# Kernel tuning notes

Hardware: AMD Instinct MI355X
Metric: run time of the kernel (lower is better)

The kernel has to match this reference:

```python
import jax, jax.numpy as jnp
import numpy as np
from jax.scipy.special import logsumexp

H = 256      # hidden_dim
K = 128      # num_clusters
SPW = 64     # states_per_word
C = K * SPW  # 8192 total states
V = 10000    # vocab
N, T = 16, 256
NEG = -1e9   # finite -inf for masking (avoids NaN rows in log_softmax)


def _residual(x, w1, b1, w2, b2):
    # ResidualLayerOld: relu(lin2(relu(lin1(x))) + x)
    h = jax.nn.relu(x @ w1.T + b1)
    return jax.nn.relu(h @ w2.T + b2 + x)


def _emb(ec, es):
    # Factored StateEmbedding: state s -> cluster_emb[s // SPW] + offset_emb[s % SPW]
    return (ec[:, None, :] + es[None, :, :]).reshape(-1, ec.shape[-1])  # [C, H]


def setup_inputs() -> dict:
    key = jax.random.key(0)
    ks = jax.random.split(key, 32)
    d = {}
    d["text"] = jax.random.randint(ks[0], (N, T), 0, V)
    d["word2cluster"] = jax.random.randint(ks[1], (V,), 0, K)
    i = 2
    for nm in ["start", "state", "next", "pre"]:
        d[nm + "_emb_c"] = jax.random.normal(ks[i], (K, H), jnp.float32) * 0.02; i += 1
        d[nm + "_emb_s"] = jax.random.normal(ks[i], (SPW, H), jnp.float32) * 0.02; i += 1
    for nm in ["start_res", "trans_res", "term_res"]:
        d[nm + "_w1"] = jax.random.normal(ks[i], (H, H), jnp.float32) / np.sqrt(H).astype(np.float32); i += 1
        d[nm + "_b1"] = jnp.zeros((H,), jnp.float32)
        d[nm + "_w2"] = jax.random.normal(ks[i], (H, H), jnp.float32) / np.sqrt(H).astype(np.float32); i += 1
        d[nm + "_b2"] = jnp.zeros((H,), jnp.float32)
    d["start_out_w"] = jax.random.normal(ks[i], (1, H), jnp.float32) / np.sqrt(H).astype(np.float32); i += 1
    d["start_out_b"] = jnp.zeros((1,), jnp.float32)
    d["term_proj_w"] = jax.random.normal(ks[i], (V, H), jnp.float32) / np.sqrt(H).astype(np.float32); i += 1
    d["term_proj_b"] = jnp.zeros((V,), jnp.float32)
    return d


def reference(text, word2cluster,
              start_emb_c, start_emb_s, state_emb_c, state_emb_s,
              next_emb_c, next_emb_s, pre_emb_c, pre_emb_s,
              start_res_w1, start_res_b1, start_res_w2, start_res_b2,
              trans_res_w1, trans_res_b1, trans_res_w2, trans_res_b2,
              term_res_w1, term_res_b1, term_res_w2, term_res_b2,
              start_out_w, start_out_b, term_proj_w, term_proj_b):
    Kc, Hd = start_emb_c.shape
    S = start_emb_s.shape[0]
    Cn = Kc * S
    Vn = word2cluster.shape[0]

    # start log-probs over states: start_mlp(start_emb).squeeze(-1).log_softmax(-1)
    se = _emb(start_emb_c, start_emb_s)                          # [C, H]
    sh = _residual(se, start_res_w1, start_res_b1, start_res_w2, start_res_b2)
    start_logp = jax.nn.log_softmax((sh @ start_out_w.T + start_out_b).squeeze(-1))  # [C]

    # transition: (trans_mlp(state_emb) @ next_state_emb.T).log_softmax(-1)
    x = _residual(_emb(state_emb_c, state_emb_s),
                  trans_res_w1, trans_res_b1, trans_res_w2, trans_res_b2)  # [C, H]
    nse = _emb(next_emb_c, next_emb_s)                           # [C, H]
    transition = jax.nn.log_softmax(x @ nse.T, axis=-1)          # [C, C]

    # emission: terminal_proj(terminal_mlp(preterminal_emb)), masked by word2state, log_softmax
    ph = _residual(_emb(pre_emb_c, pre_emb_s),
                   term_res_w1, term_res_b1, term_res_w2, term_res_b2)
    logits = ph @ term_proj_w.T + term_proj_b                    # [C, V]
    word2state = word2cluster[:, None] * S + jnp.arange(S)[None, :]  # [V, S]
    mask = jnp.zeros((Cn, Vn), bool).at[
        word2state.reshape(-1), jnp.repeat(jnp.arange(Vn), S)].set(True)
    emission = jax.nn.log_softmax(jnp.where(mask, logits, NEG), axis=-1)  # [C, V]

    # banded HMM forward DP over allowed states per word
    states = word2state[text]                                    # [N, T, S]
    emit = emission[states, text[:, :, None]]                    # [N, T, S]
    st = jnp.moveaxis(states, 1, 0)                              # [T, N, S]
    et = jnp.moveaxis(emit, 1, 0)                                # [T, N, S]
    alpha0 = start_logp[st[0]] + et[0]                           # [N, S]

    def step(alpha, inp):
        s_prev, s_cur, e_cur = inp
        tr = transition[s_prev[:, :, None], s_cur[:, None, :]]   # [N, S, S]
        alpha = logsumexp(alpha[:, :, None] + tr, axis=1) + e_cur
        return alpha, None

    alpha, _ = jax.lax.scan(step, alpha0, (st[:-1], st[1:], et[1:]))
    return logsumexp(alpha, axis=-1)                             # [N] log-evidence
```

## Files before the change

kernel.cpp:

```cpp
#include <hip/hip_runtime.h>
#include <hip/hip_bf16.h>


using u16 = unsigned short;
typedef __attribute__((ext_vector_type(8))) short bh8;
typedef __attribute__((ext_vector_type(4))) float f32x4;
typedef __attribute__((ext_vector_type(8))) unsigned short u16x8;

#define HD 256
#define TT 256
#define NB 16
#define KCL 128
#define CS 8192
#define VV 10000
#define MAXB 320
#define LOG2E 1.44269504f

__device__ __forceinline__ u16 f2bf(float v) {
  union { float f; unsigned int i; } u; u.f = v;
  unsigned int r = u.i + 0x7fffu + ((u.i >> 16) & 1u);
  return (u16)(r >> 16);
}
__device__ __forceinline__ float bf2f(u16 u) {
  union { unsigned int i; float f; } x; x.i = ((unsigned int)u) << 16; return x.f;
}
__device__ __forceinline__ void gl2lds16(const u16* g, u16* l) {
  __builtin_amdgcn_global_load_lds(
      (const __attribute__((address_space(1))) unsigned int*)g,
      (__attribute__((address_space(3))) unsigned int*)l, 16, 0, 0);
}
__device__ __forceinline__ u16x8 cvt8(const float* __restrict__ s) {
  const float4 a = *reinterpret_cast<const float4*>(s);
  const float4 b = *reinterpret_cast<const float4*>(s + 4);
  u16x8 o;
  o[0] = f2bf(a.x); o[1] = f2bf(a.y); o[2] = f2bf(a.z); o[3] = f2bf(a.w);
  o[4] = f2bf(b.x); o[5] = f2bf(b.y); o[6] = f2bf(b.z); o[7] = f2bf(b.w);
  return o;
}
__device__ __forceinline__ u16x8 add_cvt8(const float* __restrict__ s0,
                                          const float* __restrict__ s1) {
  const float4 a0 = *reinterpret_cast<const float4*>(s0);
  const float4 b0 = *reinterpret_cast<const float4*>(s0 + 4);
  const float4 a1 = *reinterpret_cast<const float4*>(s1);
  const float4 b1 = *reinterpret_cast<const float4*>(s1 + 4);
  u16x8 o;
  o[0] = f2bf(a0.x + a1.x); o[1] = f2bf(a0.y + a1.y);
  o[2] = f2bf(a0.z + a1.z); o[3] = f2bf(a0.w + a1.w);
  o[4] = f2bf(b0.x + b1.x); o[5] = f2bf(b0.y + b1.y);
  o[6] = f2bf(b0.z + b1.z); o[7] = f2bf(b0.w + b1.w);
  return o;
}


template<int LAYER>
__global__ __launch_bounds__(256) void mlp_k(
    const float* __restrict__ ec0, const float* __restrict__ es0,
    const float* __restrict__ ec1, const float* __restrict__ es1,
    const float* __restrict__ ec2, const float* __restrict__ es2,
    u16* __restrict__ H0, u16* __restrict__ H1, u16* __restrict__ H2,
    const float* __restrict__ Wf0, const float* __restrict__ Wf1,
    const float* __restrict__ Wf2,
    const float* __restrict__ bb0, const float* __restrict__ bb1, const float* __restrict__ bb2,
    const float* __restrict__ sow, float* __restrict__ hlog,
    u16* __restrict__ Xbf, u16* __restrict__ PHb,
    const int* __restrict__ w2c, int* __restrict__ offs,
    int* __restrict__ wlist, int* __restrict__ bmap,
    float* __restrict__ esum, const float* __restrict__ sob) {
  __shared__ char lds[16384];
  const int tid = threadIdx.x, lane = tid & 63, wid = tid >> 6;
  const int z = blockIdx.z;

  if (LAYER == 1 && z == 3) {
    if (blockIdx.x != 0 || blockIdx.y != 0) return;
    __shared__ int cnt[KCL], cur[KCL];
    __shared__ int wsA[2], wsB[2];
    __shared__ int totb_s;
    const int w = tid >> 6;
    if (tid < KCL) cnt[tid] = 0;
    __syncthreads();
    for (int v = tid; v < VV; v += 256) atomicAdd(&cnt[w2c[v]], 1);
    __syncthreads();
    int c = 0, x = 0;
    if (tid < KCL) {
      c = cnt[tid];
      x = c;
#pragma unroll
      for (int off = 1; off < 64; off <<= 1) {
        const int y = __shfl_up(x, off, 64);
        if (lane >= off) x += y;
      }
      if (lane == 63) wsA[w] = x;
    }
    __syncthreads();
    int nb = 0, xs = 0;
    if (tid < KCL) {
      const int base = (w == 1) ? wsA[0] : 0;
      const int excl = base + x - c;
      offs[tid] = excl;
      cur[tid] = excl;
      if (tid == KCL - 1) offs[KCL] = base + x;
      nb = (c + 63) >> 6;
      xs = nb;
#pragma unroll
      for (int off = 1; off < 64; off <<= 1) {
        const int y = __shfl_up(xs, off, 64);
        if (lane >= off) xs += y;
      }
      if (lane == 63) wsB[w] = xs;
    }
    __syncthreads();
    if (tid < KCL) {
      const int base = (w == 1) ? wsB[0] : 0;
      const int b0 = base + xs - nb;
      for (int bb = 0; bb < nb; ++bb) bmap[b0 + bb] = (tid << 8) | bb;
      if (tid == KCL - 1) totb_s = base + xs;
    }
    __syncthreads();
    const int totb = totb_s;
    for (int i = totb + tid; i < MAXB; i += 256) bmap[i] = -1;
    for (int v = tid; v < VV; v += 256) {
      const int pos = atomicAdd(&cur[w2c[v]], 1);
      wlist[pos] = v;
    }
    const float sb0 = sob[0];
    for (int i = tid; i < CS; i += 256) { esum[i] = 0.f; hlog[i] = sb0; }
    return;
  }

  const float* ec = z == 0 ? ec0 : z == 1 ? ec1 : ec2;
  const float* es = z == 0 ? es0 : z == 1 ? es1 : es2;
  u16* Hb = z == 0 ? H0 : z == 1 ? H1 : H2;
  const float* Wf = z == 0 ? Wf0 : z == 1 ? Wf1 : Wf2;
  const float* bias = z == 0 ? bb0 : z == 1 ? bb1 : bb2;

  const int rm = blockIdx.y * 64, cn = blockIdx.x * 64;
  const float* Bgf = Wf + (size_t)cn * HD;

  f32x4 acc[4];
#pragma unroll
  for (int i = 0; i < 4; ++i) acc[i] = (f32x4){0.f, 0.f, 0.f, 0.f};
  const int ra = wid * 16 + (lane & 15);
  const int rb0 = lane & 15;
  const int ko = (lane >> 4) * 8;

  for (int kc = 0; kc < HD; kc += 64) {
    if (kc) __syncthreads();
#pragma unroll
    for (int i = 0; i < 2; ++i) {
      const int c = i * 256 + tid;
      const int r = c >> 3, cb = c & 7;
      if (LAYER == 1) {
        const int grow = rm + r;
        const int krow = grow >> 6, srow = grow & 63;
        const int h0 = kc + cb * 8;
        const u16x8 v = add_cvt8(ec + krow * HD + h0, es + srow * HD + h0);
        *reinterpret_cast<u16x8*>(&lds[r * 128 + ((cb * 16) ^ ((r & 7) << 4))]) = v;
      } else {
        const int gq = cb ^ (r & 7);
        gl2lds16(Hb + (size_t)(rm + r) * HD + kc + gq * 8, (u16*)&lds[c * 16]);
      }
      const u16x8 bv = cvt8(Bgf + (size_t)r * HD + kc + cb * 8);
      *reinterpret_cast<u16x8*>(&lds[8192 + r * 128 + ((cb * 16) ^ ((r & 7) << 4))]) = bv;
    }
    __syncthreads();
#pragma unroll
    for (int kk = 0; kk < 64; kk += 32) {
      const int kb = (kk + ko) * 2;
      const bh8 af = *reinterpret_cast<const bh8*>(&lds[ra * 128 + (kb ^ ((ra & 7) << 4))]);
#pragma unroll
      for (int nj = 0; nj < 4; ++nj) {
        const int rb = nj * 16 + rb0;
        const bh8 bf = *reinterpret_cast<const bh8*>(&lds[8192 + rb * 128 + (kb ^ ((rb & 7) << 4))]);
        acc[nj] = __builtin_amdgcn_mfma_f32_16x16x32_bf16(af, bf, acc[nj], 0, 0, 0);
      }
    }
  }

  const int g = lane >> 4, c0 = lane & 15;
  float pd[4] = {0.f, 0.f, 0.f, 0.f};
#pragma unroll
  for (int nj = 0; nj < 4; ++nj) {
    const int nidx = cn + nj * 16 + c0;
    const float bv = bias[nidx];
#pragma unroll
    for (int reg = 0; reg < 4; ++reg) {
      const int midx = rm + wid * 16 + g * 4 + reg;
      float v = acc[nj][reg] + bv;
      if (LAYER == 2)
        v += ec[(midx >> 6) * HD + nidx] + es[(midx & 63) * HD + nidx];
      v = fmaxf(v, 0.f);
      if (LAYER == 1) {
        Hb[(size_t)midx * 256 + nidx] = f2bf(v);
      } else {
        if (z == 0) pd[reg] += v * sow[nidx];
        else if (z == 1) Xbf[(size_t)midx * 256 + nidx] = f2bf(v);
        else PHb[(size_t)midx * 256 + nidx] = f2bf(v);
      }
    }
  }
  if (LAYER == 2 && blockIdx.z == 0) {
#pragma unroll
    for (int off = 1; off < 16; off <<= 1)
#pragma unroll
      for (int reg = 0; reg < 4; ++reg)
        pd[reg] += __shfl_xor(pd[reg], off, 64);
    if (c0 == 0) {
#pragma unroll
      for (int reg = 0; reg < 4; ++reg)
        atomicAdd(&hlog[rm + wid * 16 + g * 4 + reg], pd[reg]);
    }
  }
}


__global__ __launch_bounds__(256) void te_k(
    const u16* __restrict__ Xbf, const float* __restrict__ nec,
    const float* __restrict__ nes,
    float* __restrict__ T12, float* __restrict__ rlse,
    const float* __restrict__ tpw, const u16* __restrict__ PHb,
    const float* __restrict__ bp,
    const int* __restrict__ offs, const int* __restrict__ wlist,
    const int* __restrict__ map,
    float* __restrict__ esum, float* __restrict__ logits_all,
    const float* __restrict__ hlog, float* __restrict__ hlseb) {
  __shared__ char lds[32768];
  const int tid = threadIdx.x, lane = tid & 63, wid = tid >> 6;
  const int rb0 = lane & 15;
  const int ko = (lane >> 4) * 8;
  const int g = lane >> 4, c0 = lane & 15;

  if (blockIdx.x == CS / 64 + MAXB) {
    __shared__ float redm[4];
    float mm = -1e30f;
    for (int i = tid; i < CS; i += 256) mm = fmaxf(mm, hlog[i]);
    for (int off = 32; off; off >>= 1) mm = fmaxf(mm, __shfl_xor(mm, off, 64));
    if (lane == 0) redm[wid] = mm;
    __syncthreads();
    const float M = fmaxf(fmaxf(redm[0], redm[1]), fmaxf(redm[2], redm[3]));
    float sx = 0.f;
    for (int i = tid; i < CS; i += 256) sx += expf(hlog[i] - M);
    for (int off = 32; off; off >>= 1) sx += __shfl_xor(sx, off, 64);
    __syncthreads();
    if (lane == 0) redm[wid] = sx;
    __syncthreads();
    if (tid == 0) hlseb[0] = M + logf(redm[0] + redm[1] + redm[2] + redm[3]);
    return;
  }

  if (blockIdx.x < CS / 64) {
    const int rm = blockIdx.x * 64;
    const int ra = wid * 16 + (lane & 15);
    f32x4 acc[12];
#pragma unroll
    for (int i = 0; i < 12; ++i) acc[i] = (f32x4){0.f, 0.f, 0.f, 0.f};

    for (int kc = 0; kc < HD; kc += 64) {
      if (kc) __syncthreads();
#pragma unroll
      for (int i = 0; i < 2; ++i) {
        const int c = i * 256 + tid;
        const int r = c >> 3, cb = c & 7;
        const int gq = cb ^ (r & 7);
        gl2lds16(Xbf + (size_t)(rm + r) * HD + kc + gq * 8, (u16*)&lds[c * 16]);
      }
#pragma unroll
      for (int i = 0; i < 6; ++i) {
        const int c = i * 256 + tid;
        const int r = c >> 3, cb = c & 7;
        const float* src = (r < KCL) ? (nec + r * HD + kc + cb * 8)
                                     : (nes + (r - KCL) * HD + kc + cb * 8);
        const u16x8 v = cvt8(src);
        *reinterpret_cast<u16x8*>(&lds[8192 + r * 128 + ((cb * 16) ^ ((r & 7) << 4))]) = v;
      }
      __syncthreads();
#pragma unroll
      for (int kk = 0; kk < 64; kk += 32) {
        const int kb = (kk + ko) * 2;
        const bh8 af = *reinterpret_cast<const bh8*>(&lds[ra * 128 + (kb ^ ((ra & 7) << 4))]);
#pragma unroll
        for (int nj = 0; nj < 12; ++nj) {
          const int rb = nj * 16 + rb0;
          const bh8 bf = *reinterpret_cast<const bh8*>(&lds[8192 + rb * 128 + (kb ^ ((rb & 7) << 4))]);
          acc[nj] = __builtin_amdgcn_mfma_f32_16x16x32_bf16(af, bf, acc[nj], 0, 0, 0);
        }
      }
    }

    float rs1[4] = {0.f, 0.f, 0.f, 0.f};
    float rs2[4] = {0.f, 0.f, 0.f, 0.f};
#pragma unroll
    for (int nj = 0; nj < 12; ++nj) {
      const int col = nj * 16 + c0;
#pragma unroll
      for (int reg = 0; reg < 4; ++reg) {
        const int row = rm + wid * 16 + g * 4 + reg;
        const float v = acc[nj][reg];
        T12[(size_t)row * 192 + col] = v;
        const float e = exp2f(v * LOG2E);
        if (nj < 8) rs1[reg] += e; else rs2[reg] += e;
      }
    }
#pragma unroll
    for (int off = 1; off < 16; off <<= 1)
#pragma unroll
      for (int reg = 0; reg < 4; ++reg) {
        rs1[reg] += __shfl_xor(rs1[reg], off, 64);
        rs2[reg] += __shfl_xor(rs2[reg], off, 64);
      }
    if (c0 == 0) {
#pragma unroll
      for (int reg = 0; reg < 4; ++reg)
        rlse[rm + wid * 16 + g * 4 + reg] = logf(rs1[reg]) + logf(rs2[reg]);
    }
    return;
  }

  const int ent = map[blockIdx.x - CS / 64];
  if (ent < 0) return;
  const int c = ent >> 8, blk = ent & 255;
  __shared__ int wid_s[64];
  const int st = offs[c], cnt = offs[c + 1] - st;
  if (tid < 64) {
    const int idx = blk * 64 + tid;
    wid_s[tid] = (idx < cnt) ? wlist[st + idx] : -1;
  }
  __syncthreads();

  f32x4 acc[4];
#pragma unroll
  for (int i = 0; i < 4; ++i) acc[i] = (f32x4){0.f, 0.f, 0.f, 0.f};
  const int ra = wid * 16 + (lane & 15);
  const u16* Bg = PHb + (size_t)(c * 64) * HD;

  for (int kc = 0; kc < HD; kc += 64) {
    if (kc) __syncthreads();
#pragma unroll
    for (int i = 0; i < 2; ++i) {
      const int cc = i * 256 + tid;
      const int r = cc >> 3, cb = cc & 7;
      const int gq = cb ^ (r & 7);
      const int wv = max(wid_s[r], 0);
      const u16x8 av = cvt8(tpw + (size_t)wv * HD + kc + cb * 8);
      *reinterpret_cast<u16x8*>(&lds[r * 128 + ((cb * 16) ^ ((r & 7) << 4))]) = av;
      gl2lds16(Bg + (size_t)r * HD + kc + gq * 8, (u16*)&lds[8192 + cc * 16]);
    }
    __syncthreads();
#pragma unroll
    for (int kk = 0; kk < 64; kk += 32) {
      const int kb = (kk + ko) * 2;
      const bh8 af = *reinterpret_cast<const bh8*>(&lds[ra * 128 + (kb ^ ((ra & 7) << 4))]);
#pragma unroll
      for (int nj = 0; nj < 4; ++nj) {
        const int rb = nj * 16 + rb0;
        const bh8 bf = *reinterpret_cast<const bh8*>(&lds[8192 + rb * 128 + (kb ^ ((rb & 7) << 4))]);
        acc[nj] = __builtin_amdgcn_mfma_f32_16x16x32_bf16(af, bf, acc[nj], 0, 0, 0);
      }
    }
  }

#pragma unroll
  for (int nj = 0; nj < 4; ++nj) {
    float se = 0.f;
#pragma unroll
    for (int reg = 0; reg < 4; ++reg) {
      const int row = wid * 16 + g * 4 + reg;
      const int w = wid_s[row];
      if (w >= 0) {
        const float lg = acc[nj][reg] + bp[w];
        logits_all[(size_t)w * 64 + nj * 16 + c0] = lg;
        se += expf(lg);
      }
    }
    se += __shfl_xor(se, 16, 64);
    se += __shfl_xor(se, 32, 64);
    if (g == 0) atomicAdd(&esum[c * 64 + nj * 16 + c0], se);
  }
}


__device__ __forceinline__ void comb4_core(
    char* lds, float* wpm,
    float sc0, float sc1, float sc2, float sc3,
    u16* node, float* dsc, int parity, int tid) {
  const int lane = tid & 63, w = tid >> 6;
  const int p = w >> 1, h = w & 1;
  const int abase = p * 16384, bbase = abase + 8192;
  const int c0 = lane & 15, g = lane >> 4;
  f32x4 a2[2][4];
#pragma unroll
  for (int mi = 0; mi < 2; ++mi)
#pragma unroll
    for (int nj = 0; nj < 4; ++nj) a2[mi][nj] = (f32x4){0.f, 0.f, 0.f, 0.f};
#pragma unroll
  for (int kk = 0; kk < 64; kk += 32) {
    const int kb = (kk + g * 8) * 2;
    bh8 af[2], bf[4];
#pragma unroll
    for (int mi = 0; mi < 2; ++mi) {
      const int ar = h * 32 + mi * 16 + c0;
      af[mi] = *reinterpret_cast<const bh8*>(&lds[abase + ar * 128 + (kb ^ ((ar & 7) << 4))]);
    }
#pragma unroll
    for (int nj = 0; nj < 4; ++nj) {
      const int br = nj * 16 + c0;
      bf[nj] = *reinterpret_cast<const bh8*>(&lds[bbase + br * 128 + (kb ^ ((br & 7) << 4))]);
    }
#pragma unroll
    for (int mi = 0; mi < 2; ++mi)
#pragma unroll
      for (int nj = 0; nj < 4; ++nj)
        a2[mi][nj] = __builtin_amdgcn_mfma_f32_16x16x32_bf16(af[mi], bf[nj], a2[mi][nj], 0, 0, 0);
  }
  float mx = 0.f;
#pragma unroll
  for (int mi = 0; mi < 2; ++mi)
#pragma unroll
    for (int nj = 0; nj < 4; ++nj)
#pragma unroll
      for (int reg = 0; reg < 4; ++reg) mx = fmaxf(mx, a2[mi][nj][reg]);
#pragma unroll
  for (int off = 1; off < 64; off <<= 1) mx = fmaxf(mx, __shfl_xor(mx, off, 64));
  if (lane == 0) wpm[w] = mx;
  __syncthreads();
  const float mp = fmaxf(wpm[p * 2], wpm[p * 2 + 1]);
  const float invp = 1.0f / mp;
#pragma unroll
  for (int mi = 0; mi < 2; ++mi)
#pragma unroll
    for (int nj = 0; nj < 4; ++nj)
#pragma unroll
      for (int reg = 0; reg < 4; ++reg) {
        const int row = h * 32 + mi * 16 + g * 4 + reg;
        const int col = nj * 16 + c0;
        const u16 val = f2bf(a2[mi][nj][reg] * invp);
        if (p == 0)
          *reinterpret_cast<u16*>(&lds[row * 128 + ((col * 2) ^ ((row & 7) << 4))]) = val;
        else
          *reinterpret_cast<u16*>(&lds[8192 + col * 128 + ((row * 2) ^ ((col & 7) << 4))]) = val;
      }
  __syncthreads();

  f32x4 acc[4];
#pragma unroll
  for (int i = 0; i < 4; ++i) acc[i] = (f32x4){0.f, 0.f, 0.f, 0.f};
  const int ra = w * 16 + c0;
#pragma unroll
  for (int kk = 0; kk < 64; kk += 32) {
    const int kb = (kk + g * 8) * 2;
    const bh8 af = *reinterpret_cast<const bh8*>(&lds[ra * 128 + (kb ^ ((ra & 7) << 4))]);
#pragma unroll
    for (int nj = 0; nj < 4; ++nj) {
      const int rb = nj * 16 + c0;
      const bh8 bf = *reinterpret_cast<const bh8*>(&lds[8192 + rb * 128 + (kb ^ ((rb & 7) << 4))]);
      acc[nj] = __builtin_amdgcn_mfma_f32_16x16x32_bf16(af, bf, acc[nj], 0, 0, 0);
    }
  }
  float mx2 = 0.f;
#pragma unroll
  for (int nj = 0; nj < 4; ++nj)
#pragma unroll
    for (int reg = 0; reg < 4; ++reg) mx2 = fmaxf(mx2, acc[nj][reg]);
#pragma unroll
  for (int off = 1; off < 64; off <<= 1) mx2 = fmaxf(mx2, __shfl_xor(mx2, off, 64));
  if (lane == 0) wpm[4 + w] = mx2;
  __syncthreads();
  const float m = fmaxf(fmaxf(wpm[4], wpm[5]), fmaxf(wpm[6], wpm[7]));
  const float inv = 1.0f / m;
  float* ftile = reinterpret_cast<float*>(lds + 16384);
#pragma unroll
  for (int nj = 0; nj < 4; ++nj)
#pragma unroll
    for (int reg = 0; reg < 4; ++reg)
      ftile[(w * 16 + g * 4 + reg) * 64 + nj * 16 + c0] = acc[nj][reg] * inv;
  __syncthreads();
  const int rr = tid >> 2, cb = (tid & 3) * 16;
  u16x8 o0, o1;
  if (parity == 0) {
#pragma unroll
    for (int e = 0; e < 8; ++e) o0[e] = f2bf(ftile[rr * 64 + cb + e]);
#pragma unroll
    for (int e = 0; e < 8; ++e) o1[e] = f2bf(ftile[rr * 64 + cb + 8 + e]);
  } else {
#pragma unroll
    for (int e = 0; e < 8; ++e) o0[e] = f2bf(ftile[(cb + e) * 64 + rr]);
#pragma unroll
    for (int e = 0; e < 8; ++e) o1[e] = f2bf(ftile[(cb + 8 + e) * 64 + rr]);
  }
  *reinterpret_cast<u16x8*>(node + rr * 64 + cb) = o0;
  *reinterpret_cast<u16x8*>(node + rr * 64 + cb + 8) = o1;
  if (tid == 0)
    *dsc = sc0 + sc1 + sc2 + sc3
         + logf(fmaxf(wpm[0], wpm[1])) + logf(fmaxf(wpm[2], wpm[3])) + logf(m);
}

__device__ __forceinline__ void comb4_stage(
    char* lds, const u16* s0, const u16* s1, const u16* s2, const u16* s3, int tid) {
  const u16* srcs[4] = {s0, s1, s2, s3};
  const int sr = tid >> 3, scb = (tid & 7) * 16;
#pragma unroll
  for (int nd = 0; nd < 4; ++nd)
#pragma unroll
    for (int rep = 0; rep < 2; ++rep) {
      const int r = rep * 32 + sr;
      const bh8 v = *reinterpret_cast<const bh8*>(srcs[nd] + r * 64 + (scb >> 1));
      *reinterpret_cast<bh8*>(&lds[nd * 8192 + r * 128 + (scb ^ ((r & 7) << 4))]) = v;
    }
  __syncthreads();
}


__global__ __launch_bounds__(256) void leafc2_k(
    const float* __restrict__ T12, const float* __restrict__ rlse,
    const float* __restrict__ lall, const float* __restrict__ esum,
    const int* __restrict__ text, const int* __restrict__ w2c,
    u16* __restrict__ dst, float* __restrict__ scd) {
  __shared__ char lds[32768];
  __shared__ float wpm[8];
  __shared__ float scl[4];
  __shared__ float ev_s[64];
  const int tid = threadIdx.x, lane = tid & 63, w = tid >> 6;
  const int n = blockIdx.x >> 6, u = blockIdx.x & 63;
  const int r = tid >> 2, cb = (tid & 3) * 16;

  for (int j = 0; j < 4; ++j) {
    const int l = 4 * u + j;
    char* slot = &lds[j * 8192];
    __syncthreads();
    if (l == 255) {
      for (int idx = tid; idx < 4096; idx += 256) {
        const int rr = idx >> 6, cc = idx & 63;
        const u16 val = (rr == cc) ? (u16)0x3F80 : (u16)0;
        *reinterpret_cast<u16*>(&slot[cc * 128 + ((rr * 2) ^ ((cc & 7) << 4))]) = val;
      }
      if (tid == 0) scl[j] = 0.f;
      continue;
    }
    const int ttv = l + 1;
    const int wcur = text[n * TT + ttv];
    const int cp = w2c[text[n * TT + ttv - 1]];
    const int cc = w2c[wcur];
    if (tid < 64)
      ev_s[tid] = lall[(size_t)wcur * 64 + tid] - logf(esum[cc * 64 + tid]);
    __syncthreads();
    const int grow = cp * 64 + r;
    const float base = T12[(size_t)grow * 192 + cc] - rlse[grow];
    const float* t2row = T12 + (size_t)grow * 192 + 128 + cb;
    float L[16];
    float mx = -1e30f;
#pragma unroll
    for (int e = 0; e < 16; ++e) {
      L[e] = base + t2row[e] + ev_s[cb + e];
      mx = fmaxf(mx, L[e]);
    }
#pragma unroll
    for (int off = 1; off < 64; off <<= 1) mx = fmaxf(mx, __shfl_xor(mx, off, 64));
    if (lane == 0) wpm[w] = mx;
    __syncthreads();
    const float m = fmaxf(fmaxf(wpm[0], wpm[1]), fmaxf(wpm[2], wpm[3]));
    if ((j & 1) == 0) {
      u16x8 o0, o1;
#pragma unroll
      for (int e = 0; e < 8; ++e) o0[e] = f2bf(exp2f((L[e] - m) * LOG2E));
#pragma unroll
      for (int e = 0; e < 8; ++e) o1[e] = f2bf(exp2f((L[8 + e] - m) * LOG2E));
      const int sw = (r & 7) << 4;
      *reinterpret_cast<u16x8*>(&slot[r * 128 + ((cb * 2) ^ sw)]) = o0;
      *reinterpret_cast<u16x8*>(&slot[r * 128 + ((cb * 2 + 16) ^ sw)]) = o1;
    } else {
#pragma unroll
      for (int e = 0; e < 16; ++e) {
        const int col = cb + e;
        const u16 val = f2bf(exp2f((L[e] - m) * LOG2E));
        *reinterpret_cast<u16*>(&slot[col * 128 + ((r * 2) ^ ((col & 7) << 4))]) = val;
      }
    }
    if (tid == 0) scl[j] = m;
  }
  __syncthreads();
  comb4_core(lds, wpm, scl[0], scl[1], scl[2], scl[3],
             dst + ((size_t)(n * 64 + u)) * 4096, &scd[n * 64 + u], u & 1, tid);
}

__global__ __launch_bounds__(256) void comb4_k(const u16* __restrict__ src,
                                               const float* __restrict__ scs,
                                               u16* __restrict__ dst,
                                               float* __restrict__ scd, int U) {
  const int n = blockIdx.x / U, u = blockIdx.x % U;
  __shared__ char lds[32768];
  __shared__ float wpm[8];
  const u16* base = src + ((size_t)(n * 4 * U + 4 * u)) * 4096;
  const float* sb = scs + n * 4 * U + 4 * u;
  comb4_stage(lds, base, base + 4096, base + 2 * 4096, base + 3 * 4096, threadIdx.x);
  comb4_core(lds, wpm, sb[0], sb[1], sb[2], sb[3],
             dst + ((size_t)(n * U + u)) * 4096, &scd[n * U + u], u & 1, threadIdx.x);
}


__global__ __launch_bounds__(256) void tail2_k(
    const u16* __restrict__ nodes, const float* __restrict__ nsc,
    u16* __restrict__ rootb,
    const float* __restrict__ hlog, const float* __restrict__ hlseb,
    const float* __restrict__ lall,
    const float* __restrict__ esum, const int* __restrict__ text,
    const int* __restrict__ w2c, float* __restrict__ out) {
  __shared__ char lds[32768];
  __shared__ float wpm[8];
  __shared__ float rsc_s;
  const int n = blockIdx.x, tid = threadIdx.x;

  const u16* src = nodes + (size_t)n * 4 * 4096;
  const float* sc = nsc + n * 4;
  u16* root = rootb + (size_t)n * 4096;
  comb4_stage(lds, src, src + 4096, src + 2 * 4096, src + 3 * 4096, tid);
  comb4_core(lds, wpm, sc[0], sc[1], sc[2], sc[3], root, &rsc_s, 0, tid);
  __syncthreads();

  if (tid < 64) {
    const int i = tid;
    const float hlse = hlseb[0];
    const int w0 = text[n * TT];
    const int cc = w2c[w0];
    const float ev = lall[(size_t)w0 * 64 + i] - logf(esum[cc * 64 + i]);
    float a0 = hlog[cc * 64 + i] - hlse + ev;
    float m0 = a0;
    for (int off = 32; off; off >>= 1) m0 = fmaxf(m0, __shfl_xor(m0, off, 64));
    const float lin = expf(a0 - m0);
    const u16* row = root + i * 64;
    float rs = 0.f;
#pragma unroll
    for (int e8 = 0; e8 < 8; ++e8) {
      const u16x8 v = *reinterpret_cast<const u16x8*>(row + e8 * 8);
#pragma unroll
      for (int e = 0; e < 8; ++e) rs += bf2f(v[e]);
    }
    float v = lin * rs;
    for (int off = 32; off; off >>= 1) v += __shfl_xor(v, off, 64);
    if (i == 0) out[n] = m0 + rsc_s + logf(v);
  }
}


extern "C" void kernel_launch(void* const* d_in, const int* in_sizes, int n_in,
                              void* d_out, int out_size, void* d_ws, size_t ws_size,
                              hipStream_t stream) {
  (void)in_sizes; (void)n_in; (void)out_size; (void)ws_size;
  const int* text = (const int*)d_in[0];
  const int* w2c  = (const int*)d_in[1];
  const float* sec = (const float*)d_in[2];
  const float* ses = (const float*)d_in[3];
  const float* stc = (const float*)d_in[4];
  const float* sts = (const float*)d_in[5];
  const float* nec = (const float*)d_in[6];
  const float* nes = (const float*)d_in[7];
  const float* pec = (const float*)d_in[8];
  const float* pes = (const float*)d_in[9];
  const float* srw1 = (const float*)d_in[10];
  const float* srb1 = (const float*)d_in[11];
  const float* srw2 = (const float*)d_in[12];
  const float* srb2 = (const float*)d_in[13];
  const float* trw1 = (const float*)d_in[14];
  const float* trb1 = (const float*)d_in[15];
  const float* trw2 = (const float*)d_in[16];
  const float* trb2 = (const float*)d_in[17];
  const float* tew1 = (const float*)d_in[18];
  const float* teb1 = (const float*)d_in[19];
  const float* tew2 = (const float*)d_in[20];
  const float* teb2 = (const float*)d_in[21];
  const float* sow = (const float*)d_in[22];
  const float* sob = (const float*)d_in[23];
  const float* tpw = (const float*)d_in[24];
  const float* tpb = (const float*)d_in[25];
  float* out = (float*)d_out;

  char* p = (char*)d_ws;
  auto carve = [&](size_t bytes) -> char* {
    char* r = p; p += (bytes + 255) & ~(size_t)255; return r;
  };
  u16* Hb0  = (u16*)carve((size_t)CS * HD * 2);
  u16* Hb1  = (u16*)carve((size_t)CS * HD * 2);
  u16* Hb2  = (u16*)carve((size_t)CS * HD * 2);
  u16* Xbf  = (u16*)carve((size_t)CS * HD * 2);
  u16* PHb  = (u16*)carve((size_t)CS * HD * 2);
  float* T12  = (float*)carve((size_t)CS * 192 * 4);
  float* hlog  = (float*)carve(CS * 4);
  float* rlse  = (float*)carve(CS * 4);
  float* hlseb = (float*)carve(256);
  int* offs    = (int*)carve((KCL + 1) * 4);
  int* wlist   = (int*)carve(VV * 4);
  int* bmap    = (int*)carve(MAXB * 4);
  float* esum  = (float*)carve(CS * 4);
  float* lall  = (float*)carve((size_t)VV * 64 * 4);
  u16*   bufA  = (u16*)carve((size_t)NB * 64 * 4096 * 2);
  u16*   bufB  = (u16*)carve((size_t)NB * 16 * 4096 * 2);
  u16*   bufC  = (u16*)carve((size_t)NB * 4 * 4096 * 2);
  u16*   rootb = (u16*)carve((size_t)NB * 4096 * 2);
  float* scA   = (float*)carve((size_t)NB * 64 * 4);
  float* scB   = (float*)carve((size_t)NB * 16 * 4);
  float* scC   = (float*)carve((size_t)NB * 4 * 4);

  mlp_k<1><<<dim3(4, 128, 4), 256, 0, stream>>>(
      sec, ses, stc, sts, pec, pes, Hb0, Hb1, Hb2,
      srw1, trw1, tew1, srb1, trb1, teb1,
      sow, hlog, nullptr, nullptr,
      w2c, offs, wlist, bmap, esum, sob);
  mlp_k<2><<<dim3(4, 128, 3), 256, 0, stream>>>(
      sec, ses, stc, sts, pec, pes, Hb0, Hb1, Hb2,
      srw2, trw2, tew2, srb2, trb2, teb2,
      sow, hlog, Xbf, PHb,
      w2c, offs, wlist, bmap, esum, sob);

  te_k<<<CS / 64 + MAXB + 1, 256, 0, stream>>>(
      Xbf, nec, nes, T12, rlse, tpw, PHb, tpb, offs, wlist, bmap, esum, lall,
      hlog, hlseb);

  leafc2_k<<<NB * 64, 256, 0, stream>>>(
      T12, rlse, lall, esum, text, w2c, bufA, scA);

  comb4_k<<<NB * 16, 256, 0, stream>>>(bufA, scA, bufB, scB, 16);
  comb4_k<<<NB * 4, 256, 0, stream>>>(bufB, scB, bufC, scC, 4);
  tail2_k<<<NB, 256, 0, stream>>>(bufC, scC, rootb, hlog, hlseb, lall, esum,
                                  text, w2c, out);
}
```

Baseline: 100.3 us.

## Factor first MLP layer through cluster and offset embeddings separately

Since the first linear layer is applied to cluster_emb + offset_emb, the product is split into W1·ec (128 rows) plus W1·es (64 rows). These 192-row partial products are precomputed in a small kernel. The second-layer kernel then rebuilds each hidden row on the fly as relu(Pc + Ps) before its GEMM. This removes the full 8192x256x256 first-layer GEMMs and the three bf16 hidden buffers, at the cost of a small 16-block launch with a low-parallelism GEMM and fp32 partial reads in the second layer.

```diff
diff --git a/kernel.cpp b/kernel.cpp
--- a/kernel.cpp
+++ b/kernel.cpp
@@ -37,41 +37,38 @@
   o[4] = f2bf(b.x); o[5] = f2bf(b.y); o[6] = f2bf(b.z); o[7] = f2bf(b.w);
   return o;
 }
-__device__ __forceinline__ u16x8 add_cvt8(const float* __restrict__ s0,
-                                          const float* __restrict__ s1) {
+__device__ __forceinline__ u16x8 relu_add_cvt8(const float* __restrict__ s0,
+                                               const float* __restrict__ s1) {
   const float4 a0 = *reinterpret_cast<const float4*>(s0);
   const float4 b0 = *reinterpret_cast<const float4*>(s0 + 4);
   const float4 a1 = *reinterpret_cast<const float4*>(s1);
   const float4 b1 = *reinterpret_cast<const float4*>(s1 + 4);
   u16x8 o;
-  o[0] = f2bf(a0.x + a1.x); o[1] = f2bf(a0.y + a1.y);
-  o[2] = f2bf(a0.z + a1.z); o[3] = f2bf(a0.w + a1.w);
-  o[4] = f2bf(b0.x + b1.x); o[5] = f2bf(b0.y + b1.y);
-  o[6] = f2bf(b0.z + b1.z); o[7] = f2bf(b0.w + b1.w);
+  o[0] = f2bf(fmaxf(a0.x + a1.x, 0.f)); o[1] = f2bf(fmaxf(a0.y + a1.y, 0.f));
+  o[2] = f2bf(fmaxf(a0.z + a1.z, 0.f)); o[3] = f2bf(fmaxf(a0.w + a1.w, 0.f));
+  o[4] = f2bf(fmaxf(b0.x + b1.x, 0.f)); o[5] = f2bf(fmaxf(b0.y + b1.y, 0.f));
+  o[6] = f2bf(fmaxf(b0.z + b1.z, 0.f)); o[7] = f2bf(fmaxf(b0.w + b1.w, 0.f));
   return o;
 }
 
 
-template<int LAYER>
-__global__ __launch_bounds__(256) void mlp_k(
+__global__ __launch_bounds__(256) void p12_k(
     const float* __restrict__ ec0, const float* __restrict__ es0,
     const float* __restrict__ ec1, const float* __restrict__ es1,
     const float* __restrict__ ec2, const float* __restrict__ es2,
-    u16* __restrict__ H0, u16* __restrict__ H1, u16* __restrict__ H2,
     const float* __restrict__ Wf0, const float* __restrict__ Wf1,
     const float* __restrict__ Wf2,
-    const float* __restrict__ bb0, const float* __restrict__ bb1, const float* __restrict__ bb2,
-    const float* __restrict__ sow, float* __restrict__ hlog,
-    u16* __restrict__ Xbf, u16* __restrict__ PHb,
+    const float* __restrict__ b0, const float* __restrict__ b1_, const float* __restrict__ b2,
+    float* __restrict__ Pb,
     const int* __restrict__ w2c, int* __restrict__ offs,
     int* __restrict__ wlist, int* __restrict__ bmap,
-    float* __restrict__ esum, const float* __restrict__ sob) {
-  __shared__ char lds[16384];
+    float* __restrict__ esum, float* __restrict__ hlog,
+    const float* __restrict__ sob) {
   const int tid = threadIdx.x, lane = tid & 63, wid = tid >> 6;
-  const int z = blockIdx.z;
-
-  if (LAYER == 1 && z == 3) {
-    if (blockIdx.x != 0 || blockIdx.y != 0) return;
+  const int z = blockIdx.y;
+
+  if (z == 3) {
+    if (blockIdx.x != 0) return;
     __shared__ int cnt[KCL], cur[KCL];
     __shared__ int wsA[2], wsB[2];
     __shared__ int totb_s;
@@ -111,8 +108,8 @@
     __syncthreads();
     if (tid < KCL) {
       const int base = (w == 1) ? wsB[0] : 0;
-      const int b0 = base + xs - nb;
-      for (int bb = 0; bb < nb; ++bb) bmap[b0 + bb] = (tid << 8) | bb;
+      const int bq = base + xs - nb;
+      for (int bb = 0; bb < nb; ++bb) bmap[bq + bb] = (tid << 8) | bb;
       if (tid == KCL - 1) totb_s = base + xs;
     }
     __syncthreads();
@@ -127,9 +124,86 @@
     return;
   }
 
+  __shared__ char lds[32768];
   const float* ec = z == 0 ? ec0 : z == 1 ? ec1 : ec2;
   const float* es = z == 0 ? es0 : z == 1 ? es1 : es2;
-  u16* Hb = z == 0 ? H0 : z == 1 ? H1 : H2;
+  const float* Wf = z == 0 ? Wf0 : z == 1 ? Wf1 : Wf2;
+  const float* bias = z == 0 ? b0 : z == 1 ? b1_ : b2;
+  float* P = Pb + (size_t)z * 192 * HD;
+
+  const int j0 = blockIdx.x * 64;
+  const int ra = wid * 16 + (lane & 15);
+  const int rb0 = lane & 15;
+  const int ko = (lane >> 4) * 8;
+  const int g = lane >> 4, c0 = lane & 15;
+
+  f32x4 acc[12];
+#pragma unroll
+  for (int i = 0; i < 12; ++i) acc[i] = (f32x4){0.f, 0.f, 0.f, 0.f};
+
+  for (int kc = 0; kc < HD; kc += 64) {
+    if (kc) __syncthreads();
+#pragma unroll
+    for (int i = 0; i < 2; ++i) {
+      const int c = i * 256 + tid;
+      const int r = c >> 3, cb = c & 7;
+      const u16x8 v = cvt8(Wf + (size_t)(j0 + r) * HD + kc + cb * 8);
+      *reinterpret_cast<u16x8*>(&lds[r * 128 + ((cb * 16) ^ ((r & 7) << 4))]) = v;
+    }
+#pragma unroll
+    for (int i = 0; i < 6; ++i) {
+      const int c = i * 256 + tid;
+      const int r = c >> 3, cb = c & 7;
+      const float* src = (r < KCL) ? (ec + r * HD + kc + cb * 8)
+                                   : (es + (r - KCL) * HD + kc + cb * 8);
+      const u16x8 v = cvt8(src);
+      *reinterpret_cast<u16x8*>(&lds[8192 + r * 128 + ((cb * 16) ^ ((r & 7) << 4))]) = v;
+    }
+    __syncthreads();
+#pragma unroll
+    for (int kk = 0; kk < 64; kk += 32) {
+      const int kb = (kk + ko) * 2;
+      const bh8 af = *reinterpret_cast<const bh8*>(&lds[ra * 128 + (kb ^ ((ra & 7) << 4))]);
+#pragma unroll
+      for (int nj = 0; nj < 12; ++nj) {
+        const int rb = nj * 16 + rb0;
+        const bh8 bf = *reinterpret_cast<const bh8*>(&lds[8192 + rb * 128 + (kb ^ ((rb & 7) << 4))]);
+        acc[nj] = __builtin_amdgcn_mfma_f32_16x16x32_bf16(af, bf, acc[nj], 0, 0, 0);
+      }
+    }
+  }
+
+#pragma unroll
+  for (int nj = 0; nj < 12; ++nj) {
+    const int r = nj * 16 + c0;
+#pragma unroll
+    for (int reg = 0; reg < 4; ++reg) {
+      const int j = j0 + wid * 16 + g * 4 + reg;
+      float v = acc[nj][reg];
+      if (r < KCL) v += bias[j];
+      P[(size_t)r * HD + j] = v;
+    }
+  }
+}
+
+
+__global__ __launch_bounds__(256) void mlp2_k(
+    const float* __restrict__ ec0, const float* __restrict__ es0,
+    const float* __restrict__ ec1, const float* __restrict__ es1,
+    const float* __restrict__ ec2, const float* __restrict__ es2,
+    const float* __restrict__ Pb,
+    const float* __restrict__ Wf0, const float* __restrict__ Wf1,
+    const float* __restrict__ Wf2,
+    const float* __restrict__ bb0, const float* __restrict__ bb1, const float* __restrict__ bb2,
+    const float* __restrict__ sow, float* __restrict__ hlog,
+    u16* __restrict__ Xbf, u16* __restrict__ PHb) {
+  __shared__ char lds[16384];
+  const int tid = threadIdx.x, lane = tid & 63, wid = tid >> 6;
+  const int z = blockIdx.z;
+
+  const float* ec = z == 0 ? ec0 : z == 1 ? ec1 : ec2;
+  const float* es = z == 0 ? es0 : z == 1 ? es1 : es2;
+  const float* Pz = Pb + (size_t)z * 192 * HD;
   const float* Wf = z == 0 ? Wf0 : z == 1 ? Wf1 : Wf2;
   const float* bias = z == 0 ? bb0 : z == 1 ? bb1 : bb2;
 
@@ -149,16 +223,12 @@
     for (int i = 0; i < 2; ++i) {
       const int c = i * 256 + tid;
       const int r = c >> 3, cb = c & 7;
-      if (LAYER == 1) {
-        const int grow = rm + r;
-        const int krow = grow >> 6, srow = grow & 63;
-        const int h0 = kc + cb * 8;
-        const u16x8 v = add_cvt8(ec + krow * HD + h0, es + srow * HD + h0);
-        *reinterpret_cast<u16x8*>(&lds[r * 128 + ((cb * 16) ^ ((r & 7) << 4))]) = v;
-      } else {
-        const int gq = cb ^ (r & 7);
-        gl2lds16(Hb + (size_t)(rm + r) * HD + kc + gq * 8, (u16*)&lds[c * 16]);
-      }
+      const int grow = rm + r;
+      const int krow = grow >> 6, srow = grow & 63;
+      const int h0 = kc + cb * 8;
+      const u16x8 v = relu_add_cvt8(Pz + (size_t)krow * HD + h0,
+                                    Pz + (size_t)(KCL + srow) * HD + h0);
+      *reinterpret_cast<u16x8*>(&lds[r * 128 + ((cb * 16) ^ ((r & 7) << 4))]) = v;
       const u16x8 bv = cvt8(Bgf + (size_t)r * HD + kc + cb * 8);
       *reinterpret_cast<u16x8*>(&lds[8192 + r * 128 + ((cb * 16) ^ ((r & 7) << 4))]) = bv;
     }
@@ -185,20 +255,15 @@
 #pragma unroll
     for (int reg = 0; reg < 4; ++reg) {
       const int midx = rm + wid * 16 + g * 4 + reg;
-      float v = acc[nj][reg] + bv;
-      if (LAYER == 2)
-        v += ec[(midx >> 6) * HD + nidx] + es[(midx & 63) * HD + nidx];
+      float v = acc[nj][reg] + bv
+              + ec[(midx >> 6) * HD + nidx] + es[(midx & 63) * HD + nidx];
       v = fmaxf(v, 0.f);
-      if (LAYER == 1) {
-        Hb[(size_t)midx * 256 + nidx] = f2bf(v);
-      } else {
-        if (z == 0) pd[reg] += v * sow[nidx];
-        else if (z == 1) Xbf[(size_t)midx * 256 + nidx] = f2bf(v);
-        else PHb[(size_t)midx * 256 + nidx] = f2bf(v);
-      }
-    }
-  }
-  if (LAYER == 2 && blockIdx.z == 0) {
+      if (z == 0) pd[reg] += v * sow[nidx];
+      else if (z == 1) Xbf[(size_t)midx * 256 + nidx] = f2bf(v);
+      else PHb[(size_t)midx * 256 + nidx] = f2bf(v);
+    }
+  }
+  if (blockIdx.z == 0) {
 #pragma unroll
     for (int off = 1; off < 16; off <<= 1)
 #pragma unroll
@@ -676,9 +741,7 @@
   auto carve = [&](size_t bytes) -> char* {
     char* r = p; p += (bytes + 255) & ~(size_t)255; return r;
   };
-  u16* Hb0  = (u16*)carve((size_t)CS * HD * 2);
-  u16* Hb1  = (u16*)carve((size_t)CS * HD * 2);
-  u16* Hb2  = (u16*)carve((size_t)CS * HD * 2);
+  float* Pb  = (float*)carve((size_t)3 * 192 * HD * 4);
   u16* Xbf  = (u16*)carve((size_t)CS * HD * 2);
   u16* PHb  = (u16*)carve((size_t)CS * HD * 2);
   float* T12  = (float*)carve((size_t)CS * 192 * 4);
@@ -698,16 +761,15 @@
   float* scB   = (float*)carve((size_t)NB * 16 * 4);
   float* scC   = (float*)carve((size_t)NB * 4 * 4);
 
-  mlp_k<1><<<dim3(4, 128, 4), 256, 0, stream>>>(
-      sec, ses, stc, sts, pec, pes, Hb0, Hb1, Hb2,
+  p12_k<<<dim3(4, 4), 256, 0, stream>>>(
+      sec, ses, stc, sts, pec, pes,
       srw1, trw1, tew1, srb1, trb1, teb1,
-      sow, hlog, nullptr, nullptr,
-      w2c, offs, wlist, bmap, esum, sob);
-  mlp_k<2><<<dim3(4, 128, 3), 256, 0, stream>>>(
-      sec, ses, stc, sts, pec, pes, Hb0, Hb1, Hb2,
+      Pb, w2c, offs, wlist, bmap, esum, hlog, sob);
+
+  mlp2_k<<<dim3(4, 128, 3), 256, 0, stream>>>(
+      sec, ses, stc, sts, pec, pes, Pb,
       srw2, trw2, tew2, srb2, trb2, teb2,
-      sow, hlog, Xbf, PHb,
-      w2c, offs, wlist, bmap, esum, sob);
+      sow, hlog, Xbf, PHb);
 
   te_k<<<CS / 64 + MAXB + 1, 256, 0, stream>>>(
       Xbf, nec, nes, T12, rlse, tpw, PHb, tpb, offs, wlist, bmap, esum, lall,
```

After: 95.44 us (median of 2 runs). -4.9%, faster.
